# Performance work log

Measured on AMD Instinct MI355X. Metric: run time of the kernel, lower is better.

The kernel has to match this reference:

```python
import jax, jax.numpy as jnp
import numpy as np

EMB_DIM = 768
N_HEAD = 12
WIN = (14, 14)  # relative_window_size; seq_len must equal 14*14=196
BATCH = 64
SEQ = WIN[0] * WIN[1]


def _relative_position_index(wh, ww):
    coords = np.stack(np.meshgrid(np.arange(wh), np.arange(ww), indexing='ij'))
    coords = coords.reshape(2, -1)
    rel = coords[:, :, None] - coords[:, None, :]          # [2, S, S]
    rel = rel.transpose(1, 2, 0).astype(np.int32)          # [S, S, 2]
    rel[:, :, 0] += wh - 1
    rel[:, :, 1] += ww - 1
    rel[:, :, 0] *= 2 * ww - 1
    return rel.sum(-1)                                     # [S, S]


def setup_inputs() -> dict:
    key = jax.random.key(0)
    ks = jax.random.split(key, 10)
    d = EMB_DIM
    std = 0.01
    x = jax.random.normal(ks[0], (BATCH, SEQ, d), dtype=jnp.float32)
    Wq = std * jax.random.normal(ks[1], (d, d), dtype=jnp.float32)
    Wk = std * jax.random.normal(ks[2], (d, d), dtype=jnp.float32)
    Wv = std * jax.random.normal(ks[3], (d, d), dtype=jnp.float32)
    Wo = std * jax.random.normal(ks[4], (d, d), dtype=jnp.float32)
    bq = jnp.zeros((d,), jnp.float32)
    bk = jnp.zeros((d,), jnp.float32)
    bv = jnp.zeros((d,), jnp.float32)
    bo = jnp.zeros((d,), jnp.float32)
    n_bias = (2 * WIN[0] - 1) * (2 * WIN[1] - 1)           # 729
    bias_table = std * jax.random.normal(ks[5], (n_bias, N_HEAD), dtype=jnp.float32)
    rel_index = jnp.asarray(_relative_position_index(WIN[0], WIN[1]))  # int32 [S,S]
    return {"x": x, "Wq": Wq, "bq": bq, "Wk": Wk, "bk": bk, "Wv": Wv,
            "bv": bv, "Wo": Wo, "bo": bo, "bias_table": bias_table,
            "rel_index": rel_index}


def reference(x, Wq, bq, Wk, bk, Wv, bv, Wo, bo, bias_table, rel_index):
    B, S, D = x.shape
    H = N_HEAD
    pd = D // H  # projection_dim

    def split_heads(t):
        return t.reshape(B, S, H, pd).transpose(0, 2, 1, 3)  # [B,H,S,pd]

    q = split_heads(x @ Wq + bq)
    k = split_heads(x @ Wk + bk)
    v = split_heads(x @ Wv + bv)

    # scores: [B,H,S,S], scaled by sqrt(projection_dim) as in the source
    score = jnp.einsum('bhqd,bhkd->bhqk', q, k) / jnp.sqrt(jnp.float32(pd))

    # Swin-style relative position bias: gather [S*S] rows -> [1,H,S,S]
    bias = bias_table[rel_index.reshape(-1)].reshape(S, S, H)
    bias = bias.transpose(2, 0, 1)[None]
    score = score + bias

    weight = jax.nn.softmax(score, axis=-1)
    out = jnp.einsum('bhqk,bhkd->bhqd', weight, v)          # [B,H,S,pd]
    out = out.transpose(0, 2, 1, 3).reshape(B, S, D)
    return out @ Wo + bo
```

## Files before the change

### kernel.cpp

```cpp
#include <hip/hip_runtime.h>
#include <hip/hip_bf16.h>


typedef __bf16 bf16x8 __attribute__((ext_vector_type(8)));
typedef __bf16 bf16x4 __attribute__((ext_vector_type(4)));
typedef float  f32x4  __attribute__((ext_vector_type(4)));

#define MROWS 12544
#define DDIM  768
#define NHEAD 12
#define SEQ   196
#define VSTR  232

static __device__ __forceinline__ f32x4 MFMA(bf16x8 a, bf16x8 b, f32x4 c) {
    return __builtin_amdgcn_mfma_f32_16x16x32_bf16(a, b, c, 0, 0, 0);
}

static __device__ __forceinline__ void gload16(const __bf16* g, __bf16* l) {
    __builtin_amdgcn_global_load_lds(
        (const __attribute__((address_space(1))) void*)(g),
        (__attribute__((address_space(3))) void*)(l),
        16, 0, 0);
}

__global__ __launch_bounds__(256) void f2b(const float* __restrict__ in,
                                           __bf16* __restrict__ out) {
    size_t i = ((size_t)blockIdx.x * 256 + threadIdx.x) * 8;
    f32x4 a = *(const f32x4*)&in[i];
    f32x4 b = *(const f32x4*)&in[i + 4];
    bf16x8 o;
    o[0] = (__bf16)a[0]; o[1] = (__bf16)a[1]; o[2] = (__bf16)a[2]; o[3] = (__bf16)a[3];
    o[4] = (__bf16)b[0]; o[5] = (__bf16)b[1]; o[6] = (__bf16)b[2]; o[7] = (__bf16)b[3];
    *(bf16x8*)&out[i] = o;
}

__global__ __launch_bounds__(256) void wtrans(const float* __restrict__ W0, const float* __restrict__ W1,
                                              const float* __restrict__ W2, const float* __restrict__ W3,
                                              __bf16* __restrict__ T0, __bf16* __restrict__ T1,
                                              __bf16* __restrict__ T2, __bf16* __restrict__ T3) {
    const float* Ws[4] = {W0, W1, W2, W3};
    __bf16*      Ts[4] = {T0, T1, T2, T3};
    const float* W = Ws[blockIdx.z];
    __bf16*      T = Ts[blockIdx.z];
    const float s = (blockIdx.z == 0) ? 0.125f : 1.0f;
    __shared__ __bf16 t[32][33];
    int k0 = blockIdx.x * 32, n0 = blockIdx.y * 32;
    int c = threadIdx.x & 31, r = threadIdx.x >> 5;
#pragma unroll
    for (int i = 0; i < 4; ++i)
        t[r + i * 8][c] = (__bf16)(W[(size_t)(k0 + r + i * 8) * DDIM + n0 + c] * s);
    __syncthreads();
#pragma unroll
    for (int i = 0; i < 4; ++i)
        T[(size_t)(n0 + r + i * 8) * DDIM + k0 + c] = t[c][r + i * 8];
}

__global__ __launch_bounds__(256) void bias_pre(const float* __restrict__ table,
                                                const int* __restrict__ rel,
                                                __bf16* __restrict__ biasH) {
    int i = blockIdx.x * 256 + threadIdx.x;
    if (i < NHEAD * SEQ * SEQ) {
        int h = i / (SEQ * SEQ), qk = i - h * (SEQ * SEQ);
        biasH[i] = (__bf16)table[rel[qk] * NHEAD + h];
    }
}

template <typename OutT, int NMAT>
__global__ __launch_bounds__(512, 2) void gemm8p(const __bf16* __restrict__ A,
                                                 const __bf16* __restrict__ Bt,
                                                 const float* __restrict__ bz0,
                                                 const float* __restrict__ bz1,
                                                 const float* __restrict__ bz2,
                                                 OutT* __restrict__ Cz0,
                                                 OutT* __restrict__ Cz1,
                                                 OutT* __restrict__ Cz2,
                                                 int nbn) {
    __shared__ __bf16 As[3][256 * 64];
    __shared__ __bf16 Bs[2][256 * 64];

    const int nwg = gridDim.x, orig = blockIdx.x;
    const int qq = nwg >> 3, r8 = nwg & 7, xcd = orig & 7, lin = orig >> 3;
    const int wg = (xcd < r8 ? xcd * (qq + 1) : r8 * (qq + 1) + (xcd - r8) * qq) + lin;
    const int bm = wg / nbn, bn = wg - bm * nbn;
    const int m0 = bm * 256, n0g = bn * 256;

    const int tid = threadIdx.x, w = tid >> 6, l = tid & 63;
    const int lr = l & 15, lg = l >> 4;
    const int wrow = (w >> 2) * 128;
    const int wcol = (w & 3) * 64;

    const int srow = w * 8 + (l >> 3);
    const int scol = ((l & 7) ^ ((l >> 3) & 7)) * 8;
    const __bf16* gA = A  + (size_t)(m0 + srow) * DDIM + scol;
    const __bf16* gB = Bt + (size_t)(n0g + srow) * DDIM + scol;

#define STAGE_A(slot, h, kt)                                                      \
    do {                                                                          \
        gload16(gA + ((h) * 128 + 0) * DDIM + (kt) * 64,                          \
                &As[slot][(h) * 8192 + 0 + w * 512]);                             \
        gload16(gA + ((h) * 128 + 64) * DDIM + (kt) * 64,                         \
                &As[slot][(h) * 8192 + 4096 + w * 512]);                          \
    } while (0)
#define STAGE_B(slot, h, kt)                                                      \
    do {                                                                          \
        gload16(gB + ((h) * 128 + 0) * DDIM + (kt) * 64,                          \
                &Bs[slot][(h) * 8192 + 0 + w * 512]);                             \
        gload16(gB + ((h) * 128 + 64) * DDIM + (kt) * 64,                         \
                &Bs[slot][(h) * 8192 + 4096 + w * 512]);                          \
    } while (0)

#define AF(slot, mf, ks)                                                          \
    (*(const bf16x8*)&As[slot][(w >> 2) * 8192 + ((mf) * 16 + lr) * 64 +          \
                              ((((ks) * 4 + lg) ^ (lr & 7))) * 8])
#define BF(slot, nf, ks)                                                          \
    (*(const bf16x8*)&Bs[slot][((w & 3) >> 1) * 8192 +                            \
                              ((w & 1) * 64 + (nf) * 16 + lr) * 64 +              \
                              ((((ks) * 4 + lg) ^ (lr & 7))) * 8])

    f32x4 acc[8][4];
#pragma unroll
    for (int i = 0; i < 8; ++i)
#pragma unroll
        for (int j = 0; j < 4; ++j) acc[i][j] = (f32x4){0.f, 0.f, 0.f, 0.f};

    bf16x8 a0, a1, a2, a3;
    bf16x8 bfr00, bfr01, bfr10, bfr11, bfr20, bfr21, bfr30, bfr31;

#define DSLOAD_A(slot, mf0)                                                       \
    a0 = AF(slot, mf0, 0); a1 = AF(slot, mf0, 1);                                 \
    a2 = AF(slot, (mf0) + 1, 0); a3 = AF(slot, (mf0) + 1, 1);
#define DSLOAD_B(slot)                                                            \
    bfr00 = BF(slot, 0, 0); bfr01 = BF(slot, 0, 1);                               \
    bfr10 = BF(slot, 1, 0); bfr11 = BF(slot, 1, 1);                               \
    bfr20 = BF(slot, 2, 0); bfr21 = BF(slot, 2, 1);                               \
    bfr30 = BF(slot, 3, 0); bfr31 = BF(slot, 3, 1);
#define BARRIER_IN()                                                              \
    __builtin_amdgcn_sched_barrier(0);                                            \
    __builtin_amdgcn_s_barrier();                                                 \
    asm volatile("s_waitcnt lgkmcnt(0)" ::: "memory");                            \
    __builtin_amdgcn_sched_barrier(0);                                            \
    __builtin_amdgcn_s_setprio(1);
#define BARRIER_OUT()                                                             \
    __builtin_amdgcn_s_setprio(0);                                                \
    __builtin_amdgcn_sched_barrier(0);                                            \
    __builtin_amdgcn_s_barrier();                                                 \
    __builtin_amdgcn_sched_barrier(0);
#define MFMACL(mf0)                                                               \
    acc[mf0][0] = MFMA(a0, bfr00, acc[mf0][0]);                                   \
    acc[mf0][0] = MFMA(a1, bfr01, acc[mf0][0]);                                   \
    acc[(mf0) + 1][0] = MFMA(a2, bfr00, acc[(mf0) + 1][0]);                       \
    acc[(mf0) + 1][0] = MFMA(a3, bfr01, acc[(mf0) + 1][0]);                       \
    acc[mf0][1] = MFMA(a0, bfr10, acc[mf0][1]);                                   \
    acc[mf0][1] = MFMA(a1, bfr11, acc[mf0][1]);                                   \
    acc[(mf0) + 1][1] = MFMA(a2, bfr10, acc[(mf0) + 1][1]);                       \
    acc[(mf0) + 1][1] = MFMA(a3, bfr11, acc[(mf0) + 1][1]);                       \
    acc[mf0][2] = MFMA(a0, bfr20, acc[mf0][2]);                                   \
    acc[mf0][2] = MFMA(a1, bfr21, acc[mf0][2]);                                   \
    acc[(mf0) + 1][2] = MFMA(a2, bfr20, acc[(mf0) + 1][2]);                       \
    acc[(mf0) + 1][2] = MFMA(a3, bfr21, acc[(mf0) + 1][2]);                       \
    acc[mf0][3] = MFMA(a0, bfr30, acc[mf0][3]);                                   \
    acc[mf0][3] = MFMA(a1, bfr31, acc[mf0][3]);                                   \
    acc[(mf0) + 1][3] = MFMA(a2, bfr30, acc[(mf0) + 1][3]);                       \
    acc[(mf0) + 1][3] = MFMA(a3, bfr31, acc[(mf0) + 1][3]);

    STAGE_A(0, 0, 0); STAGE_A(0, 1, 0); STAGE_B(0, 0, 0); STAGE_B(0, 1, 0);
    STAGE_A(1, 0, 1); STAGE_A(1, 1, 1); STAGE_B(1, 0, 1); STAGE_B(1, 1, 1);
    asm volatile("s_waitcnt vmcnt(8)" ::: "memory");
    __builtin_amdgcn_s_barrier();
    __builtin_amdgcn_sched_barrier(0);

#pragma unroll
    for (int i = 0; i < 6; ++i) {
        const int s0 = (2 * i) % 3, s1 = (2 * i + 1) % 3, s2 = (2 * i + 2) % 3;
        DSLOAD_A(s0, 0); DSLOAD_B(0);
        if (i < 5) STAGE_A(s2, 0, 2 * i + 2);
        BARRIER_IN(); MFMACL(0); BARRIER_OUT();
        DSLOAD_A(s0, 2);
        if (i < 5) STAGE_A(s2, 1, 2 * i + 2);
        BARRIER_IN(); MFMACL(2); BARRIER_OUT();
        DSLOAD_A(s0, 4);
        if (i < 5) STAGE_B(0, 0, 2 * i + 2);
        BARRIER_IN(); MFMACL(4); BARRIER_OUT();
        DSLOAD_A(s0, 6);
        if (i < 5) {
            STAGE_B(0, 1, 2 * i + 2);
            asm volatile("s_waitcnt vmcnt(8)" ::: "memory");
        } else {
            asm volatile("s_waitcnt vmcnt(0)" ::: "memory");
        }
        BARRIER_IN(); MFMACL(6); BARRIER_OUT();
        DSLOAD_A(s1, 0); DSLOAD_B(1);
        if (i < 5) STAGE_A(s0, 0, 2 * i + 3);
        BARRIER_IN(); MFMACL(0); BARRIER_OUT();
        DSLOAD_A(s1, 2);
        if (i < 5) STAGE_A(s0, 1, 2 * i + 3);
        BARRIER_IN(); MFMACL(2); BARRIER_OUT();
        DSLOAD_A(s1, 4);
        if (i < 5) STAGE_B(1, 0, 2 * i + 3);
        BARRIER_IN(); MFMACL(4); BARRIER_OUT();
        DSLOAD_A(s1, 6);
        if (i < 5) {
            STAGE_B(1, 1, 2 * i + 3);
            asm volatile("s_waitcnt vmcnt(8)" ::: "memory");
        }
        BARRIER_IN(); MFMACL(6); BARRIER_OUT();
    }

    const int mat = (NMAT == 1) ? 0 : (n0g / DDIM);
    const int colbase = n0g - mat * DDIM + wcol;
    const float* bz = (mat == 0) ? bz0 : (mat == 1 ? bz1 : bz2);
    OutT* Cc = (mat == 0) ? Cz0 : (mat == 1 ? Cz1 : Cz2);
    const float bsc = (NMAT == 3 && mat == 0) ? 0.125f : 1.0f;
#pragma unroll
    for (int nf = 0; nf < 4; ++nf) {
        const int col = colbase + nf * 16 + lr;
        const float bb = bz[col] * bsc;
#pragma unroll
        for (int mf = 0; mf < 8; ++mf) {
            const int row = m0 + wrow + mf * 16 + lg * 4;
#pragma unroll
            for (int r2 = 0; r2 < 4; ++r2)
                Cc[(size_t)(row + r2) * DDIM + col] = (OutT)(acc[mf][nf][r2] + bb);
        }
    }
#undef STAGE_A
#undef STAGE_B
#undef AF
#undef BF
#undef DSLOAD_A
#undef DSLOAD_B
#undef BARRIER_IN
#undef BARRIER_OUT
#undef MFMACL
}

__global__ __launch_bounds__(512, 1) void attn_kernel(const __bf16* __restrict__ Qg,
                                                      const __bf16* __restrict__ Kg,
                                                      const __bf16* __restrict__ Vg,
                                                      const __bf16* __restrict__ biasH,
                                                      __bf16* __restrict__ Og) {
    __shared__ __bf16 Ksm[196 * 64];
    __shared__ __bf16 Vts[64 * VSTR];
    __shared__ __bf16 Psm[13 * 16 * VSTR];

    const int b = blockIdx.x, h = blockIdx.y;
    const int tid = threadIdx.x, w = tid >> 6, l = tid & 63;
    const int lr = l & 15, lg = l >> 4;
    const size_t base = (size_t)(b * SEQ) * DDIM + h * 64;
    const __bf16* Kb = Kg + base;
    const __bf16* Vb = Vg + base;
    const __bf16* Qb = Qg + base;
    const __bf16* bh = biasH + (size_t)h * (SEQ * SEQ);

    for (int c = tid; c < SEQ * 8; c += 512) {
        int kk = c >> 3, ch = c & 7;
        *(bf16x8*)&Ksm[kk * 64 + ((ch ^ (kk & 7)) << 3)] =
            *(const bf16x8*)&Kb[(size_t)kk * DDIM + (ch << 3)];
    }
    for (int c = tid; c < SEQ * 8; c += 512) {
        int kk = c >> 3, a = c & 7, d8 = a << 3;
        bf16x8 vv = *(const bf16x8*)&Vb[(size_t)kk * DDIM + d8];
#pragma unroll
        for (int jj = 0; jj < 8; ++jj) {
            int j = (jj + a) & 7;
            Vts[(d8 + j) * VSTR + kk] = vv[j];
        }
    }
    for (int c = tid; c < 64 * 28; c += 512)
        Vts[(c / 28) * VSTR + SEQ + (c % 28)] = (__bf16)0.f;
    for (int c = tid; c < 13 * 16 * 16; c += 512) {
        int buf = c >> 8, rr = (c >> 4) & 15, cc = c & 15;
        Psm[(buf * 16 + rr) * VSTR + 208 + cc] = (__bf16)0.f;
    }
    __syncthreads();

#define KF(row, ch) (*(const bf16x8*)&Ksm[(row) * 64 + (((ch) ^ ((row) & 7)) << 3)])

    const int qtA = w;
    const int qtB = 8 + w;
    const bool hasB = (qtB < 13);
    __bf16* PA = &Psm[(qtA * 16) * VSTR];
    __bf16* PB = &Psm[(min(qtB, 12) * 16) * VSTR];

    const int qA = qtA * 16 + lr;
    const int qB = qtB * 16 + lr;
    const int qrowB = min(qB, SEQ - 1);

    bf16x8 bqA0 = *(const bf16x8*)&Qb[(size_t)qA * DDIM + lg * 8];
    bf16x8 bqA1 = *(const bf16x8*)&Qb[(size_t)qA * DDIM + 32 + lg * 8];
    bf16x8 bqB0 = *(const bf16x8*)&Qb[(size_t)qrowB * DDIM + lg * 8];
    bf16x8 bqB1 = *(const bf16x8*)&Qb[(size_t)qrowB * DDIM + 32 + lg * 8];

    float psA = 0.f, psB = 0.f;
#pragma unroll
    for (int tt = 0; tt < 13; ++tt) {
        const int krow = (tt < 12) ? (tt * 16 + lr) : min(tt * 16 + lr, SEQ - 1);
        bf16x8 kf0 = KF(krow, lg);
        bf16x8 kf1 = KF(krow, 4 + lg);
        f32x4 aA = {0.f, 0.f, 0.f, 0.f};
        aA = MFMA(kf0, bqA0, aA);
        aA = MFMA(kf1, bqA1, aA);
        f32x4 aB = {0.f, 0.f, 0.f, 0.f};
        aB = MFMA(kf0, bqB0, aB);
        aB = MFMA(kf1, bqB1, aB);
        const bool val4 = (tt < 12) || (lg == 0);
        bf16x4 b4A = *(const bf16x4*)&bh[(size_t)qA * SEQ + tt * 16 + lg * 4];
        bf16x4 b4B = *(const bf16x4*)&bh[(size_t)qrowB * SEQ + tt * 16 + lg * 4];
        bf16x4 pkA, pkB;
#pragma unroll
        for (int r = 0; r < 4; ++r) {
            float pA_ = val4 ? __expf(aA[r] + (float)b4A[r]) : 0.f;
            float pB_ = val4 ? __expf(aB[r] + (float)b4B[r]) : 0.f;
            psA += pA_;
            psB += pB_;
            pkA[r] = (__bf16)pA_;
            pkB[r] = (__bf16)pB_;
        }
        *(bf16x4*)&PA[lr * VSTR + tt * 16 + lg * 4] = pkA;
        if (hasB) *(bf16x4*)&PB[lr * VSTR + tt * 16 + lg * 4] = pkB;
    }
    psA += __shfl_xor(psA, 16); psA += __shfl_xor(psA, 32);
    psB += __shfl_xor(psB, 16); psB += __shfl_xor(psB, 32);

    f32x4 oaA[4], oaB[4];
#pragma unroll
    for (int i = 0; i < 4; ++i) {
        oaA[i] = (f32x4){0.f, 0.f, 0.f, 0.f};
        oaB[i] = (f32x4){0.f, 0.f, 0.f, 0.f};
    }
    __builtin_amdgcn_s_setprio(1);
#pragma unroll
    for (int kt = 0; kt < 7; ++kt) {
        bf16x8 pfA = *(const bf16x8*)&PA[lr * VSTR + kt * 32 + lg * 8];
        bf16x8 pfB = *(const bf16x8*)&PB[lr * VSTR + kt * 32 + lg * 8];
#pragma unroll
        for (int nt = 0; nt < 4; ++nt) {
            bf16x8 vf = *(const bf16x8*)&Vts[(nt * 16 + lr) * VSTR + kt * 32 + lg * 8];
            oaA[nt] = MFMA(vf, pfA, oaA[nt]);
            oaB[nt] = MFMA(vf, pfB, oaB[nt]);
        }
    }
    __builtin_amdgcn_s_setprio(0);

    const float invA = 1.f / psA;
    {
#pragma unroll
        for (int nt = 0; nt < 4; ++nt) {
            bf16x4 ok;
#pragma unroll
            for (int r = 0; r < 4; ++r) ok[r] = (__bf16)(oaA[nt][r] * invA);
            *(bf16x4*)&Og[(size_t)(b * SEQ + qA) * DDIM + h * 64 + nt * 16 + lg * 4] = ok;
        }
    }
    if (qB < SEQ) {
        const float invB = 1.f / psB;
#pragma unroll
        for (int nt = 0; nt < 4; ++nt) {
            bf16x4 ok;
#pragma unroll
            for (int r = 0; r < 4; ++r) ok[r] = (__bf16)(oaB[nt][r] * invB);
            *(bf16x4*)&Og[(size_t)(b * SEQ + qB) * DDIM + h * 64 + nt * 16 + lg * 4] = ok;
        }
    }
#undef KF
}

extern "C" void kernel_launch(void* const* d_in, const int* in_sizes, int n_in,
                              void* d_out, int out_size, void* d_ws, size_t ws_size,
                              hipStream_t stream) {
    const float* x     = (const float*)d_in[0];
    const float* Wq    = (const float*)d_in[1];
    const float* bq    = (const float*)d_in[2];
    const float* Wk    = (const float*)d_in[3];
    const float* bk    = (const float*)d_in[4];
    const float* Wv    = (const float*)d_in[5];
    const float* bv    = (const float*)d_in[6];
    const float* Wo    = (const float*)d_in[7];
    const float* bo    = (const float*)d_in[8];
    const float* table = (const float*)d_in[9];
    const int*   rel   = (const int*)d_in[10];
    float* out = (float*)d_out;

    char* ws = (char*)d_ws;
    auto alloc = [&](size_t bytes) {
        char* p = ws;
        ws += (bytes + 255) & ~(size_t)255;
        return p;
    };
    const size_t mat = (size_t)MROWS * DDIM * sizeof(__bf16);
    __bf16* xb    = (__bf16*)alloc(mat);
    __bf16* Tqkv  = (__bf16*)alloc((size_t)3 * DDIM * DDIM * 2);
    __bf16* To    = (__bf16*)alloc((size_t)DDIM * DDIM * 2);
    __bf16* Qb    = (__bf16*)alloc(mat);
    __bf16* Kb    = (__bf16*)alloc(mat);
    __bf16* Vb    = (__bf16*)alloc(mat);
    __bf16* AO    = (__bf16*)alloc(mat);
    __bf16* biasH = (__bf16*)alloc((size_t)NHEAD * SEQ * SEQ * 2 + 1024);

    f2b<<<dim3(4704), 256, 0, stream>>>(x, xb);
    wtrans<<<dim3(24, 24, 4), 256, 0, stream>>>(Wq, Wk, Wv, Wo,
                                                Tqkv, Tqkv + (size_t)DDIM * DDIM,
                                                Tqkv + (size_t)2 * DDIM * DDIM, To);
    bias_pre<<<dim3(1801), 256, 0, stream>>>(table, rel, biasH);

    gemm8p<__bf16, 3><<<dim3(441), 512, 0, stream>>>(xb, Tqkv, bq, bk, bv,
                                                     Qb, Kb, Vb, 9);
    attn_kernel<<<dim3(64, 12), 512, 0, stream>>>(Qb, Kb, Vb, biasH, AO);
    gemm8p<float, 1><<<dim3(147), 512, 0, stream>>>(AO, To, bo, bo, bo,
                                                    out, out, out, 3);
}
```

Measured before the change: 141.4 us.

## Merge prep kernels, pad bias table with mask, add half-tile output GEMM

Combines the x conversion, weight transpose and bias gather into one launch to remove two kernel launches. The relative-bias table is padded to a stride of 208 and filled with a large negative value past the sequence end, which drops the per-element validity check in attention. The output projection moves to a new GEMM with 128-row tiles and triple-buffered B, launching 294 workgroups instead of 147 to fill more CUs. In exchange the bias buffer grows and there is a second GEMM kernel to maintain.

Result: no change. 141.0 us (-0.2%).

```diff
diff --git a/kernel.cpp b/kernel.cpp
--- a/kernel.cpp
+++ b/kernel.cpp
@@ -10,6 +10,7 @@
 #define DDIM  768
 #define NHEAD 12
 #define SEQ   196
+#define BSTR  208
 #define VSTR  232
 
 static __device__ __forceinline__ f32x4 MFMA(bf16x8 a, bf16x8 b, f32x4 c) {
@@ -23,57 +24,60 @@
         16, 0, 0);
 }
 
-__global__ __launch_bounds__(256) void f2b(const float* __restrict__ in,
-                                           __bf16* __restrict__ out) {
-    size_t i = ((size_t)blockIdx.x * 256 + threadIdx.x) * 8;
-    f32x4 a = *(const f32x4*)&in[i];
-    f32x4 b = *(const f32x4*)&in[i + 4];
-    bf16x8 o;
-    o[0] = (__bf16)a[0]; o[1] = (__bf16)a[1]; o[2] = (__bf16)a[2]; o[3] = (__bf16)a[3];
-    o[4] = (__bf16)b[0]; o[5] = (__bf16)b[1]; o[6] = (__bf16)b[2]; o[7] = (__bf16)b[3];
-    *(bf16x8*)&out[i] = o;
-}
-
-__global__ __launch_bounds__(256) void wtrans(const float* __restrict__ W0, const float* __restrict__ W1,
-                                              const float* __restrict__ W2, const float* __restrict__ W3,
-                                              __bf16* __restrict__ T0, __bf16* __restrict__ T1,
-                                              __bf16* __restrict__ T2, __bf16* __restrict__ T3) {
-    const float* Ws[4] = {W0, W1, W2, W3};
-    __bf16*      Ts[4] = {T0, T1, T2, T3};
-    const float* W = Ws[blockIdx.z];
-    __bf16*      T = Ts[blockIdx.z];
-    const float s = (blockIdx.z == 0) ? 0.125f : 1.0f;
-    __shared__ __bf16 t[32][33];
-    int k0 = blockIdx.x * 32, n0 = blockIdx.y * 32;
-    int c = threadIdx.x & 31, r = threadIdx.x >> 5;
-#pragma unroll
-    for (int i = 0; i < 4; ++i)
-        t[r + i * 8][c] = (__bf16)(W[(size_t)(k0 + r + i * 8) * DDIM + n0 + c] * s);
-    __syncthreads();
-#pragma unroll
-    for (int i = 0; i < 4; ++i)
-        T[(size_t)(n0 + r + i * 8) * DDIM + k0 + c] = t[c][r + i * 8];
-}
-
-__global__ __launch_bounds__(256) void bias_pre(const float* __restrict__ table,
-                                                const int* __restrict__ rel,
-                                                __bf16* __restrict__ biasH) {
-    int i = blockIdx.x * 256 + threadIdx.x;
-    if (i < NHEAD * SEQ * SEQ) {
-        int h = i / (SEQ * SEQ), qk = i - h * (SEQ * SEQ);
-        biasH[i] = (__bf16)table[rel[qk] * NHEAD + h];
-    }
-}
-
-template <typename OutT, int NMAT>
+__global__ __launch_bounds__(256) void prep_all(const float* __restrict__ x, __bf16* __restrict__ xb,
+                                                const float* __restrict__ W0, const float* __restrict__ W1,
+                                                const float* __restrict__ W2, const float* __restrict__ W3,
+                                                __bf16* __restrict__ T0, __bf16* __restrict__ T1,
+                                                __bf16* __restrict__ T2, __bf16* __restrict__ T3,
+                                                const float* __restrict__ table, const int* __restrict__ rel,
+                                                __bf16* __restrict__ biasHP) {
+    const int bid = blockIdx.x, tid = threadIdx.x;
+    if (bid < 4704) {
+        size_t i = ((size_t)bid * 256 + tid) * 8;
+        f32x4 a = *(const f32x4*)&x[i];
+        f32x4 b = *(const f32x4*)&x[i + 4];
+        bf16x8 o;
+        o[0] = (__bf16)a[0]; o[1] = (__bf16)a[1]; o[2] = (__bf16)a[2]; o[3] = (__bf16)a[3];
+        o[4] = (__bf16)b[0]; o[5] = (__bf16)b[1]; o[6] = (__bf16)b[2]; o[7] = (__bf16)b[3];
+        *(bf16x8*)&xb[i] = o;
+    } else if (bid < 7008) {
+        const int z = bid - 4704;
+        const int which = z / 576, rr = z % 576;
+        const int kx = rr / 24, ny = rr % 24;
+        const float* Ws[4] = {W0, W1, W2, W3};
+        __bf16*      Ts[4] = {T0, T1, T2, T3};
+        const float* W = Ws[which];
+        __bf16*      T = Ts[which];
+        const float s = (which == 0) ? 0.125f : 1.0f;
+        __shared__ __bf16 t[32][33];
+        int k0 = kx * 32, n0 = ny * 32;
+        int c = tid & 31, r = tid >> 5;
+#pragma unroll
+        for (int i = 0; i < 4; ++i)
+            t[r + i * 8][c] = (__bf16)(W[(size_t)(k0 + r + i * 8) * DDIM + n0 + c] * s);
+        __syncthreads();
+#pragma unroll
+        for (int i = 0; i < 4; ++i)
+            T[(size_t)(n0 + r + i * 8) * DDIM + k0 + c] = t[c][r + i * 8];
+    } else {
+        int i = (bid - 7008) * 256 + tid;
+        if (i < NHEAD * SEQ * BSTR) {
+            int h = i / (SEQ * BSTR), rr = i - h * (SEQ * BSTR);
+            int q = rr / BSTR, k = rr - q * BSTR;
+            biasHP[i] = (k < SEQ) ? (__bf16)table[rel[q * SEQ + k] * NHEAD + h]
+                                  : (__bf16)(-10000.f);
+        }
+    }
+}
+
 __global__ __launch_bounds__(512, 2) void gemm8p(const __bf16* __restrict__ A,
                                                  const __bf16* __restrict__ Bt,
                                                  const float* __restrict__ bz0,
                                                  const float* __restrict__ bz1,
                                                  const float* __restrict__ bz2,
-                                                 OutT* __restrict__ Cz0,
-                                                 OutT* __restrict__ Cz1,
-                                                 OutT* __restrict__ Cz2,
+                                                 __bf16* __restrict__ Cz0,
+                                                 __bf16* __restrict__ Cz1,
+                                                 __bf16* __restrict__ Cz2,
                                                  int nbn) {
     __shared__ __bf16 As[3][256 * 64];
     __shared__ __bf16 Bs[2][256 * 64];
@@ -108,7 +112,6 @@
         gload16(gB + ((h) * 128 + 64) * DDIM + (kt) * 64,                         \
                 &Bs[slot][(h) * 8192 + 4096 + w * 512]);                          \
     } while (0)
-
 #define AF(slot, mf, ks)                                                          \
     (*(const bf16x8*)&As[slot][(w >> 2) * 8192 + ((mf) * 16 + lr) * 64 +          \
                               ((((ks) * 4 + lg) ^ (lr & 7))) * 8])
@@ -206,11 +209,11 @@
         BARRIER_IN(); MFMACL(6); BARRIER_OUT();
     }
 
-    const int mat = (NMAT == 1) ? 0 : (n0g / DDIM);
+    const int mat = n0g / DDIM;
     const int colbase = n0g - mat * DDIM + wcol;
     const float* bz = (mat == 0) ? bz0 : (mat == 1 ? bz1 : bz2);
-    OutT* Cc = (mat == 0) ? Cz0 : (mat == 1 ? Cz1 : Cz2);
-    const float bsc = (NMAT == 3 && mat == 0) ? 0.125f : 1.0f;
+    __bf16* Cc = (mat == 0) ? Cz0 : (mat == 1 ? Cz1 : Cz2);
+    const float bsc = (mat == 0) ? 0.125f : 1.0f;
 #pragma unroll
     for (int nf = 0; nf < 4; ++nf) {
         const int col = colbase + nf * 16 + lr;
@@ -220,7 +223,7 @@
             const int row = m0 + wrow + mf * 16 + lg * 4;
 #pragma unroll
             for (int r2 = 0; r2 < 4; ++r2)
-                Cc[(size_t)(row + r2) * DDIM + col] = (OutT)(acc[mf][nf][r2] + bb);
+                Cc[(size_t)(row + r2) * DDIM + col] = (__bf16)(acc[mf][nf][r2] + bb);
         }
     }
 #undef STAGE_A
@@ -229,15 +232,147 @@
 #undef BF
 #undef DSLOAD_A
 #undef DSLOAD_B
+#undef MFMACL
+}
+
+__global__ __launch_bounds__(512, 2) void gemm8p_h(const __bf16* __restrict__ A,
+                                                   const __bf16* __restrict__ Bt,
+                                                   const float* __restrict__ bz,
+                                                   float* __restrict__ C,
+                                                   int nbn) {
+    __shared__ __bf16 As[3][128 * 64];
+    __shared__ __bf16 Bs[3][256 * 64];
+
+    const int nwg = gridDim.x, orig = blockIdx.x;
+    const int qq = nwg >> 3, r8 = nwg & 7, xcd = orig & 7, lin = orig >> 3;
+    const int wg = (xcd < r8 ? xcd * (qq + 1) : r8 * (qq + 1) + (xcd - r8) * qq) + lin;
+    const int bm = wg / nbn, bn = wg - bm * nbn;
+    const int m0 = bm * 128, n0g = bn * 256;
+
+    const int tid = threadIdx.x, w = tid >> 6, l = tid & 63;
+    const int lr = l & 15, lg = l >> 4;
+    const int wrow = (w >> 2) * 64;
+    const int wcol = (w & 3) * 64;
+
+    const int srow = w * 8 + (l >> 3);
+    const int scol = ((l & 7) ^ ((l >> 3) & 7)) * 8;
+    const __bf16* gA = A  + (size_t)(m0 + srow) * DDIM + scol;
+    const __bf16* gB = Bt + (size_t)(n0g + srow) * DDIM + scol;
+
+#define STAGE_AH(slot, kt)                                                        \
+    do {                                                                          \
+        gload16(gA + 0 * DDIM + (kt) * 64,  &As[slot][0 + w * 512]);              \
+        gload16(gA + 64 * DDIM + (kt) * 64, &As[slot][4096 + w * 512]);           \
+    } while (0)
+#define STAGE_BH(slot, h, kt)                                                     \
+    do {                                                                          \
+        gload16(gB + ((h) * 128 + 0) * DDIM + (kt) * 64,                          \
+                &Bs[slot][(h) * 8192 + 0 + w * 512]);                             \
+        gload16(gB + ((h) * 128 + 64) * DDIM + (kt) * 64,                         \
+                &Bs[slot][(h) * 8192 + 4096 + w * 512]);                          \
+    } while (0)
+#define AFH(slot, mf, ks)                                                         \
+    (*(const bf16x8*)&As[slot][(w >> 2) * 4096 + ((mf) * 16 + lr) * 64 +          \
+                              ((((ks) * 4 + lg) ^ (lr & 7))) * 8])
+#define BFH(slot, nf, ks)                                                         \
+    (*(const bf16x8*)&Bs[slot][((w & 3) >> 1) * 8192 +                            \
+                              ((w & 1) * 64 + (nf) * 16 + lr) * 64 +              \
+                              ((((ks) * 4 + lg) ^ (lr & 7))) * 8])
+
+    f32x4 acc[4][4];
+#pragma unroll
+    for (int i = 0; i < 4; ++i)
+#pragma unroll
+        for (int j = 0; j < 4; ++j) acc[i][j] = (f32x4){0.f, 0.f, 0.f, 0.f};
+
+    bf16x8 a0, a1, a2, a3;
+    bf16x8 bfr00, bfr01, bfr10, bfr11, bfr20, bfr21, bfr30, bfr31;
+
+#define DSLOAD_AH(slot, mf0)                                                      \
+    a0 = AFH(slot, mf0, 0); a1 = AFH(slot, mf0, 1);                               \
+    a2 = AFH(slot, (mf0) + 1, 0); a3 = AFH(slot, (mf0) + 1, 1);
+#define DSLOAD_BH(slot)                                                           \
+    bfr00 = BFH(slot, 0, 0); bfr01 = BFH(slot, 0, 1);                             \
+    bfr10 = BFH(slot, 1, 0); bfr11 = BFH(slot, 1, 1);                             \
+    bfr20 = BFH(slot, 2, 0); bfr21 = BFH(slot, 2, 1);                             \
+    bfr30 = BFH(slot, 3, 0); bfr31 = BFH(slot, 3, 1);
+#define MFMACLH(mf0)                                                              \
+    acc[mf0][0] = MFMA(a0, bfr00, acc[mf0][0]);                                   \
+    acc[mf0][0] = MFMA(a1, bfr01, acc[mf0][0]);                                   \
+    acc[(mf0) + 1][0] = MFMA(a2, bfr00, acc[(mf0) + 1][0]);                       \
+    acc[(mf0) + 1][0] = MFMA(a3, bfr01, acc[(mf0) + 1][0]);                       \
+    acc[mf0][1] = MFMA(a0, bfr10, acc[mf0][1]);                                   \
+    acc[mf0][1] = MFMA(a1, bfr11, acc[mf0][1]);                                   \
+    acc[(mf0) + 1][1] = MFMA(a2, bfr10, acc[(mf0) + 1][1]);                       \
+    acc[(mf0) + 1][1] = MFMA(a3, bfr11, acc[(mf0) + 1][1]);                       \
+    acc[mf0][2] = MFMA(a0, bfr20, acc[mf0][2]);                                   \
+    acc[mf0][2] = MFMA(a1, bfr21, acc[mf0][2]);                                   \
+    acc[(mf0) + 1][2] = MFMA(a2, bfr20, acc[(mf0) + 1][2]);                       \
+    acc[(mf0) + 1][2] = MFMA(a3, bfr21, acc[(mf0) + 1][2]);                       \
+    acc[mf0][3] = MFMA(a0, bfr30, acc[mf0][3]);                                   \
+    acc[mf0][3] = MFMA(a1, bfr31, acc[mf0][3]);                                   \
+    acc[(mf0) + 1][3] = MFMA(a2, bfr30, acc[(mf0) + 1][3]);                       \
+    acc[(mf0) + 1][3] = MFMA(a3, bfr31, acc[(mf0) + 1][3]);
+
+    STAGE_AH(0, 0); STAGE_BH(0, 0, 0); STAGE_BH(0, 1, 0);
+    STAGE_AH(1, 1); STAGE_BH(1, 0, 1); STAGE_BH(1, 1, 1);
+    asm volatile("s_waitcnt vmcnt(6)" ::: "memory");
+    __builtin_amdgcn_s_barrier();
+    __builtin_amdgcn_sched_barrier(0);
+
+#pragma unroll
+    for (int i = 0; i < 6; ++i) {
+        const int s0 = (2 * i) % 3, s1 = (2 * i + 1) % 3, s2 = (2 * i + 2) % 3;
+        DSLOAD_AH(s0, 0); DSLOAD_BH(s0);
+        if (i < 5) STAGE_AH(s2, 2 * i + 2);
+        BARRIER_IN(); MFMACLH(0); BARRIER_OUT();
+        DSLOAD_AH(s0, 2);
+        if (i < 5) {
+            STAGE_BH(s2, 0, 2 * i + 2); STAGE_BH(s2, 1, 2 * i + 2);
+            asm volatile("s_waitcnt vmcnt(6)" ::: "memory");
+        } else {
+            asm volatile("s_waitcnt vmcnt(0)" ::: "memory");
+        }
+        BARRIER_IN(); MFMACLH(2); BARRIER_OUT();
+        DSLOAD_AH(s1, 0); DSLOAD_BH(s1);
+        if (i < 5) STAGE_AH(s0, 2 * i + 3);
+        BARRIER_IN(); MFMACLH(0); BARRIER_OUT();
+        DSLOAD_AH(s1, 2);
+        if (i < 5) {
+            STAGE_BH(s0, 0, 2 * i + 3); STAGE_BH(s0, 1, 2 * i + 3);
+            asm volatile("s_waitcnt vmcnt(6)" ::: "memory");
+        }
+        BARRIER_IN(); MFMACLH(2); BARRIER_OUT();
+    }
+
+    const int colbase = n0g + wcol;
+#pragma unroll
+    for (int nf = 0; nf < 4; ++nf) {
+        const int col = colbase + nf * 16 + lr;
+        const float bb = bz[col];
+#pragma unroll
+        for (int mf = 0; mf < 4; ++mf) {
+            const int row = m0 + wrow + mf * 16 + lg * 4;
+#pragma unroll
+            for (int r2 = 0; r2 < 4; ++r2)
+                C[(size_t)(row + r2) * DDIM + col] = acc[mf][nf][r2] + bb;
+        }
+    }
+#undef STAGE_AH
+#undef STAGE_BH
+#undef AFH
+#undef BFH
+#undef DSLOAD_AH
+#undef DSLOAD_BH
+#undef MFMACLH
 #undef BARRIER_IN
 #undef BARRIER_OUT
-#undef MFMACL
 }
 
 __global__ __launch_bounds__(512, 1) void attn_kernel(const __bf16* __restrict__ Qg,
                                                       const __bf16* __restrict__ Kg,
                                                       const __bf16* __restrict__ Vg,
-                                                      const __bf16* __restrict__ biasH,
+                                                      const __bf16* __restrict__ biasHP,
                                                       __bf16* __restrict__ Og) {
     __shared__ __bf16 Ksm[196 * 64];
     __shared__ __bf16 Vts[64 * VSTR];
@@ -250,7 +385,7 @@
     const __bf16* Kb = Kg + base;
     const __bf16* Vb = Vg + base;
     const __bf16* Qb = Qg + base;
-    const __bf16* bh = biasH + (size_t)h * (SEQ * SEQ);
+    const __bf16* bh = biasHP + (size_t)h * (SEQ * BSTR);
 
     for (int c = tid; c < SEQ * 8; c += 512) {
         int kk = c >> 3, ch = c & 7;
@@ -303,14 +438,13 @@
         f32x4 aB = {0.f, 0.f, 0.f, 0.f};
         aB = MFMA(kf0, bqB0, aB);
         aB = MFMA(kf1, bqB1, aB);
-        const bool val4 = (tt < 12) || (lg == 0);
-        bf16x4 b4A = *(const bf16x4*)&bh[(size_t)qA * SEQ + tt * 16 + lg * 4];
-        bf16x4 b4B = *(const bf16x4*)&bh[(size_t)qrowB * SEQ + tt * 16 + lg * 4];
+        bf16x4 b4A = *(const bf16x4*)&bh[(size_t)qA * BSTR + tt * 16 + lg * 4];
+        bf16x4 b4B = *(const bf16x4*)&bh[(size_t)qrowB * BSTR + tt * 16 + lg * 4];
         bf16x4 pkA, pkB;
 #pragma unroll
         for (int r = 0; r < 4; ++r) {
-            float pA_ = val4 ? __expf(aA[r] + (float)b4A[r]) : 0.f;
-            float pB_ = val4 ? __expf(aB[r] + (float)b4B[r]) : 0.f;
+            float pA_ = __expf(aA[r] + (float)b4A[r]);
+            float pB_ = __expf(aB[r] + (float)b4B[r]);
             psA += pA_;
             psB += pB_;
             pkA[r] = (__bf16)pA_;
@@ -395,17 +529,14 @@
     __bf16* Kb    = (__bf16*)alloc(mat);
     __bf16* Vb    = (__bf16*)alloc(mat);
     __bf16* AO    = (__bf16*)alloc(mat);
-    __bf16* biasH = (__bf16*)alloc((size_t)NHEAD * SEQ * SEQ * 2 + 1024);
-
-    f2b<<<dim3(4704), 256, 0, stream>>>(x, xb);
-    wtrans<<<dim3(24, 24, 4), 256, 0, stream>>>(Wq, Wk, Wv, Wo,
-                                                Tqkv, Tqkv + (size_t)DDIM * DDIM,
-                                                Tqkv + (size_t)2 * DDIM * DDIM, To);
-    bias_pre<<<dim3(1801), 256, 0, stream>>>(table, rel, biasH);
-
-    gemm8p<__bf16, 3><<<dim3(441), 512, 0, stream>>>(xb, Tqkv, bq, bk, bv,
-                                                     Qb, Kb, Vb, 9);
-    attn_kernel<<<dim3(64, 12), 512, 0, stream>>>(Qb, Kb, Vb, biasH, AO);
-    gemm8p<float, 1><<<dim3(147), 512, 0, stream>>>(AO, To, bo, bo, bo,
-                                                    out, out, out, 3);
-}
+    __bf16* biasHP = (__bf16*)alloc((size_t)NHEAD * SEQ * BSTR * 2);
+
+    prep_all<<<dim3(8919), 256, 0, stream>>>(x, xb, Wq, Wk, Wv, Wo,
+                                             Tqkv, Tqkv + (size_t)DDIM * DDIM,
+                                             Tqkv + (size_t)2 * DDIM * DDIM, To,
+                                             table, rel, biasHP);
+
+    gemm8p<<<dim3(441), 512, 0, stream>>>(xb, Tqkv, bq, bk, bv, Qb, Kb, Vb, 9);
+    attn_kernel<<<dim3(64, 12), 512, 0, stream>>>(Qb, Kb, Vb, biasHP, AO);
+    gemm8p_h<<<dim3(294), 512, 0, stream>>>(AO, To, bo, out, 3);
+}
```
